# Kernel tuning notes

Measured on AMD Instinct MI355X. Metric: run time of the kernel, lower is better.

Reference implementation:

```python
import jax, jax.numpy as jnp
import numpy as np

EMBED_DIM = 256
N_LEVELS = 4
N_HEADS = 8
N_POINTS = 4
HEAD_DIM = EMBED_DIM // N_HEADS
N_QUERIES = 8192
BATCH = 2
LEVEL_SHAPES = np.array([[128, 128], [64, 64], [32, 32], [16, 16]], dtype=np.int32)
HMAX, WMAX = 128, 128
EPS = 1e-5


def setup_inputs() -> dict:
    key = jax.random.key(0)
    ks = jax.random.split(key, 10)
    scale = 1.0 / np.sqrt(EMBED_DIM)
    query = jax.random.normal(ks[0], (N_QUERIES, EMBED_DIM), jnp.float32)
    xy_reference_points = jax.random.uniform(ks[1], (N_QUERIES, 2), jnp.float32, 0.05, 0.95)
    val = jax.random.normal(ks[2], (BATCH, HMAX, WMAX, N_LEVELS, EMBED_DIM), jnp.float32)
    # zero outside each level's valid support (mimics sparse COO: absent entries read as 0)
    hh = jnp.arange(HMAX)[:, None, None]
    ww = jnp.arange(WMAX)[None, :, None]
    lh = jnp.asarray(LEVEL_SHAPES[:, 0])[None, None, :]
    lw = jnp.asarray(LEVEL_SHAPES[:, 1])[None, None, :]
    mask = ((hh < lh) & (ww < lw)).astype(jnp.float32)
    stacked_value_tensors = val * mask[None, :, :, :, None]
    return {
        "query": query,
        "xy_reference_points": xy_reference_points,
        "stacked_value_tensors": stacked_value_tensors,
        "W_off": (jax.random.normal(ks[3], (EMBED_DIM, N_LEVELS * N_POINTS * N_HEADS * 2)) * scale * 0.1).astype(jnp.float32),
        "b_off": (jax.random.normal(ks[4], (N_LEVELS * N_POINTS * N_HEADS * 2,)) * 0.5).astype(jnp.float32),
        "W_attn": (jax.random.normal(ks[5], (EMBED_DIM, N_LEVELS * N_POINTS * N_HEADS)) * scale).astype(jnp.float32),
        "b_attn": jnp.zeros((N_LEVELS * N_POINTS * N_HEADS,), jnp.float32),
        "W_out": (jax.random.normal(ks[6], (EMBED_DIM, EMBED_DIM)) * scale).astype(jnp.float32),
        "b_out": jnp.zeros((EMBED_DIM,), jnp.float32),
        "batch_offsets": jnp.array([0, N_QUERIES // 2], jnp.int32),
        "spatial_shapes": jnp.asarray(LEVEL_SHAPES, jnp.int32),
    }


def reference(query, xy_reference_points, stacked_value_tensors, W_off, b_off,
              W_attn, b_attn, W_out, b_out, batch_offsets, spatial_shapes):
    Q = query.shape[0]
    # sampling offsets & attention weights (torch Linear with W stored [in,out])
    off = (query @ W_off + b_off).reshape(Q, N_LEVELS, N_POINTS, N_HEADS, 2)
    aw = (query @ W_attn + b_attn).reshape(Q, N_LEVELS * N_POINTS, N_HEADS)
    aw = jax.nn.softmax(aw, axis=1).reshape(Q, N_LEVELS, N_POINTS, N_HEADS)
    # sampling locations: sigmoid(inverse_sigmoid(ref) + offsets), then map (0,1)->(-1,1)
    r = jnp.clip(xy_reference_points, 0.0, 1.0)
    inv = jnp.log(jnp.clip(r, EPS, 1.0) / jnp.clip(1.0 - r, EPS, 1.0))
    loc = jax.nn.sigmoid(inv[:, None, None, None, :] + off) * 2.0 - 1.0  # (Q,L,P,H,2)
    # per-query batch index from batch_offsets (start index per batch element)
    bidx = jnp.searchsorted(batch_offsets, jnp.arange(Q), side="right") - 1  # (Q,)
    b = bidx[:, None, None, None]
    h_sz = spatial_shapes[:, 0].astype(loc.dtype)[None, :, None, None]
    w_sz = spatial_shapes[:, 1].astype(loc.dtype)[None, :, None, None]
    x = ((loc[..., 0] + 1.0) * w_sz - 1.0) / 2.0  # (Q,L,P,H)
    y = ((loc[..., 1] + 1.0) * h_sz - 1.0) / 2.0
    x0 = jnp.floor(x).astype(jnp.int32); x1 = x0 + 1
    y0 = jnp.floor(y).astype(jnp.int32); y1 = y0 + 1
    wcap = (spatial_shapes[:, 1] - 1).astype(jnp.int32)[None, :, None, None]
    hcap = (spatial_shapes[:, 0] - 1).astype(jnp.int32)[None, :, None, None]
    x0 = jnp.clip(x0, 0, wcap); x1 = jnp.clip(x1, 0, wcap)
    y0 = jnp.clip(y0, 0, hcap); y1 = jnp.clip(y1, 0, hcap)
    x0f = x0.astype(x.dtype); x1f = x1.astype(x.dtype)
    y0f = y0.astype(y.dtype); y1f = y1.astype(y.dtype)
    wa = (x1f - x) * (y1f - y)  # pairs with (x0,y0), as in source
    wb = (x1f - x) * (y - y0f)  # (x0,y1)
    wc = (x - x0f) * (y1f - y)  # (x1,y0)
    wd = (x - x0f) * (y - y0f)  # (x1,y1)
    V = stacked_value_tensors.reshape(BATCH, HMAX, WMAX, N_LEVELS, N_HEADS, HEAD_DIM)
    l = jnp.arange(N_LEVELS)[None, :, None, None]
    h = jnp.arange(N_HEADS)[None, None, None, :]
    # NOTE: source indexes (batch, x, y, level, head) -> x indexes the height dim; levels are square
    def g(xi, yi):
        return V[b, xi, yi, l, h]  # (Q,L,P,H,HEAD_DIM)
    sampled = (wa[..., None] * g(x0, y0) + wb[..., None] * g(x0, y1)
               + wc[..., None] * g(x1, y0) + wd[..., None] * g(x1, y1))
    out = jnp.einsum("qlphd,qlph->qhd", sampled, aw).reshape(Q, EMBED_DIM)
    return out @ W_out + b_out
```

## Files before the change

kernel.cpp:

```cpp
#include <hip/hip_runtime.h>
#include <math.h>

#define ED      256
#define NL      4
#define NH      8
#define NP      4
#define HD      32
#define HMAX    128
#define WMAX    128
#define NLP     16
#define NC      128
#define NOFF_AW 384
#define QPB     4
#define BSTRIDE (HMAX*WMAX*NL*ED)
#define XSTRIDE (WMAX*NL*ED)
#define YSTRIDE (NL*ED)
#define RPB     21760
#define PBC     (RPB*256)

typedef __attribute__((ext_vector_type(8))) __fp16   f16x8;
typedef __attribute__((ext_vector_type(4))) __fp16   f16x4;
typedef __attribute__((ext_vector_type(4))) float    f32x4;

__constant__ int LBASE_ROW[4] = {0, 16384, 20480, 21504};

__global__ __launch_bounds__(1024) void msda_prep_kernel(
    const float* __restrict__ V,
    const float* __restrict__ W_off,
    const float* __restrict__ W_attn,
    const float* __restrict__ W_out,
    __fp16* __restrict__ Vc,
    __fp16* __restrict__ WcatT,
    __fp16* __restrict__ WoutT,
    int nb, int nCompact)
{
    const int bid = blockIdx.x;
    const int t   = threadIdx.x;

    if (bid < nCompact) {
        const int r    = bid * 16 + (t >> 6);
        const int lane = t & 63;
        const int h    = lane >> 3;
        const int j4   = lane & 7;
        const int total_rows = nb * RPB;
        if (r < total_rows) {
            const int b  = r / RPB;
            const int rr = r - b * RPB;
            int l;
            if (rr < 16384)      { l = 0; }
            else if (rr < 20480) { l = 1; }
            else if (rr < 21504) { l = 2; }
            else                 { l = 3; }
            const int pos = rr - LBASE_ROW[l];
            const int lsh = 7 - l;
            const int xi  = pos >> lsh;
            const int yi  = pos & ((1 << lsh) - 1);
            const int plane32 = (1 << (2 * lsh)) * 32;
            const float4 src = *(const float4*)&V[(size_t)b * BSTRIDE +
                (size_t)xi * XSTRIDE + (size_t)yi * YSTRIDE + l * ED +
                h * HD + j4 * 4];
            f16x4 d;
            d[0] = (__fp16)src.x; d[1] = (__fp16)src.y;
            d[2] = (__fp16)src.z; d[3] = (__fp16)src.w;
            const size_t dst = (size_t)b * PBC + (size_t)LBASE_ROW[l] * 256 +
                               (size_t)h * plane32 + (size_t)pos * 32 + j4 * 4;
            *(f16x4*)&Vc[dst] = d;
        }
    } else {
        const int idx = (bid - nCompact) * 1024 + t;
        const int t2 = NOFF_AW * ED;
        const int t3 = ED * ED;
        if (idx < t2) {
            int c = idx >> 8, e = idx & 255;
            float v = (c < ED) ? W_off[e * ED + c] : W_attn[e * NC + (c - ED)];
            WcatT[idx] = (__fp16)v;
        } else if (idx < t2 + t3) {
            int i = idx - t2;
            int c = i >> 8, e = i & 255;
            WoutT[i] = (__fp16)W_out[e * ED + c];
        }
    }
}

__global__ __launch_bounds__(256) void gemm_f16_kernel(
    const float*  __restrict__ A,
    const __fp16* __restrict__ BT,
    const float* __restrict__ bias0,
    const float* __restrict__ bias1,
    float* __restrict__ C,
    int M, int NTOT, int bias_split)
{
    const int wave = threadIdx.x >> 6;
    const int lane = threadIdx.x & 63;
    const int gw   = blockIdx.x * 4 + wave;
    const int ngroups = NTOT >> 6;
    const int mg = gw / ngroups, ng = gw % ngroups;
    const int m16 = mg * 16, n64 = ng * 64;
    if (m16 >= M) return;

    const int mrow = lane & 15;
    const int quad = lane >> 4;

    const float4* Arow = (const float4*)(A + (size_t)(m16 + mrow) * 256 + quad * 8);
    const f16x8* B0 = (const f16x8*)(BT + (size_t)(n64 +  0 + mrow) * 256 + quad * 8);
    const f16x8* B1 = (const f16x8*)(BT + (size_t)(n64 + 16 + mrow) * 256 + quad * 8);
    const f16x8* B2 = (const f16x8*)(BT + (size_t)(n64 + 32 + mrow) * 256 + quad * 8);
    const f16x8* B3 = (const f16x8*)(BT + (size_t)(n64 + 48 + mrow) * 256 + quad * 8);

    f32x4 acc0 = {0.f,0.f,0.f,0.f}, acc1 = acc0, acc2 = acc0, acc3 = acc0;
    #pragma unroll
    for (int kb = 0; kb < 8; ++kb) {
        float4 a0 = Arow[kb * 8 + 0];
        float4 a1 = Arow[kb * 8 + 1];
        float av[8] = {a0.x, a0.y, a0.z, a0.w, a1.x, a1.y, a1.z, a1.w};
        f16x8 ah, al;
        #pragma unroll
        for (int j = 0; j < 8; ++j) {
            __fp16 h = (__fp16)av[j];
            ah[j] = h;
            al[j] = (__fp16)(av[j] - (float)h);
        }
        f16x8 b0 = B0[kb * 4], b1 = B1[kb * 4], b2 = B2[kb * 4], b3 = B3[kb * 4];
        acc0 = __builtin_amdgcn_mfma_f32_16x16x32_f16(ah, b0, acc0, 0, 0, 0);
        acc1 = __builtin_amdgcn_mfma_f32_16x16x32_f16(ah, b1, acc1, 0, 0, 0);
        acc2 = __builtin_amdgcn_mfma_f32_16x16x32_f16(ah, b2, acc2, 0, 0, 0);
        acc3 = __builtin_amdgcn_mfma_f32_16x16x32_f16(ah, b3, acc3, 0, 0, 0);
        acc0 = __builtin_amdgcn_mfma_f32_16x16x32_f16(al, b0, acc0, 0, 0, 0);
        acc1 = __builtin_amdgcn_mfma_f32_16x16x32_f16(al, b1, acc1, 0, 0, 0);
        acc2 = __builtin_amdgcn_mfma_f32_16x16x32_f16(al, b2, acc2, 0, 0, 0);
        acc3 = __builtin_amdgcn_mfma_f32_16x16x32_f16(al, b3, acc3, 0, 0, 0);
    }

    const int col = lane & 15;
    f32x4 accs[4] = {acc0, acc1, acc2, acc3};
    #pragma unroll
    for (int i = 0; i < 4; ++i) {
        int n = n64 + i * 16 + col;
        float b = (n < bias_split) ? bias0[n] : bias1[n - bias_split];
        #pragma unroll
        for (int r = 0; r < 4; ++r) {
            int row = m16 + quad * 4 + r;
            C[(size_t)row * NTOT + n] = accs[i][r] + b;
        }
    }
}

__global__ __launch_bounds__(256) void gemm_ff16_kernel(
    const __fp16* __restrict__ A,
    const __fp16* __restrict__ BT,
    const float* __restrict__ bias,
    float* __restrict__ C,
    int M, int NTOT)
{
    const int wave = threadIdx.x >> 6;
    const int lane = threadIdx.x & 63;
    const int gw   = blockIdx.x * 4 + wave;
    const int ngroups = NTOT >> 6;
    const int mg = gw / ngroups, ng = gw % ngroups;
    const int m16 = mg * 16, n64 = ng * 64;
    if (m16 >= M) return;

    const int mrow = lane & 15;
    const int quad = lane >> 4;

    const f16x8* Arow = (const f16x8*)(A + (size_t)(m16 + mrow) * 256 + quad * 8);
    const f16x8* B0 = (const f16x8*)(BT + (size_t)(n64 +  0 + mrow) * 256 + quad * 8);
    const f16x8* B1 = (const f16x8*)(BT + (size_t)(n64 + 16 + mrow) * 256 + quad * 8);
    const f16x8* B2 = (const f16x8*)(BT + (size_t)(n64 + 32 + mrow) * 256 + quad * 8);
    const f16x8* B3 = (const f16x8*)(BT + (size_t)(n64 + 48 + mrow) * 256 + quad * 8);

    f32x4 acc0 = {0.f,0.f,0.f,0.f}, acc1 = acc0, acc2 = acc0, acc3 = acc0;
    #pragma unroll
    for (int kb = 0; kb < 8; ++kb) {
        f16x8 af = Arow[kb * 4];
        acc0 = __builtin_amdgcn_mfma_f32_16x16x32_f16(af, B0[kb * 4], acc0, 0, 0, 0);
        acc1 = __builtin_amdgcn_mfma_f32_16x16x32_f16(af, B1[kb * 4], acc1, 0, 0, 0);
        acc2 = __builtin_amdgcn_mfma_f32_16x16x32_f16(af, B2[kb * 4], acc2, 0, 0, 0);
        acc3 = __builtin_amdgcn_mfma_f32_16x16x32_f16(af, B3[kb * 4], acc3, 0, 0, 0);
    }

    const int col = lane & 15;
    f32x4 accs[4] = {acc0, acc1, acc2, acc3};
    #pragma unroll
    for (int i = 0; i < 4; ++i) {
        int n = n64 + i * 16 + col;
        float b = bias[n];
        #pragma unroll
        for (int r = 0; r < 4; ++r) {
            int row = m16 + quad * 4 + r;
            C[(size_t)row * NTOT + n] = accs[i][r] + b;
        }
    }
}

__global__ __launch_bounds__(256) void msda_sample_kernel(
    const float*  __restrict__ refp,
    const __fp16* __restrict__ Vc,
    const float*  __restrict__ off_aw,
    const int*    __restrict__ batch_off,
    int n_batch,
    __fp16* __restrict__ out_pre,
    int q_total)
{
    __shared__ float  law[QPB][NC];
    __shared__ float2 sminv[QPB][NH];
    __shared__ float2 sref[QPB];
    __shared__ int2   soff[QPB][NC];
    __shared__ float4 swt[QPB][NC];

    const int t  = threadIdx.x;
    const int q0 = blockIdx.x * QPB;

    {
        const int s = t >> 6, c = t & 63;
        const float* row = off_aw + (size_t)(q0 + s) * NOFF_AW + ED;
        law[s][c]      = row[c];
        law[s][c + 64] = row[c + 64];
    }
    __syncthreads();

    if (t < QPB * NH) {
        const int s = t >> 3, h = t & 7;
        float m = -1e30f;
        #pragma unroll
        for (int lp = 0; lp < NLP; ++lp) m = fmaxf(m, law[s][lp * NH + h]);
        float sum = 0.f;
        #pragma unroll
        for (int lp = 0; lp < NLP; ++lp) sum += __expf(law[s][lp * NH + h] - m);
        sminv[s][h] = make_float2(m, 1.f / sum);
    } else if (t < QPB * NH + QPB) {
        const int s = t - QPB * NH;
        const int qid = q0 + s;
        float rx = refp[qid * 2 + 0], ry = refp[qid * 2 + 1];
        rx = fminf(fmaxf(rx, 0.f), 1.f);
        ry = fminf(fmaxf(ry, 0.f), 1.f);
        float ivx = __logf(fmaxf(rx, 1e-5f) / fmaxf(1.f - rx, 1e-5f));
        float ivy = __logf(fmaxf(ry, 1e-5f) / fmaxf(1.f - ry, 1e-5f));
        sref[s] = make_float2(ivx, ivy);
    }
    __syncthreads();

    {
        const int s = t >> 6;
        const int qid = q0 + s;
        int b = 0;
        for (int i = 1; i < n_batch; ++i)
            if (batch_off[i] <= qid) b = i;
        const int cb = b * PBC;
        const float2 iv = sref[s];
        const float* offrow = off_aw + (size_t)qid * NOFF_AW;

        #pragma unroll
        for (int half = 0; half < 2; ++half) {
            const int c = (t & 63) + half * 64;
            const int l = c >> 5;
            const int lsh = 7 - l;
            const int sz  = 1 << lsh;
            const int cap = sz - 1;
            const int h = c & 7;
            const int plane32 = (sz * sz) << 5;

            const float2 mi = sminv[s][h];
            const float a = __expf(law[s][c] - mi.x) * mi.y;

            const float ox = offrow[c * 2 + 0], oy = offrow[c * 2 + 1];
            float lx = 2.f / (1.f + __expf(-(iv.x + ox))) - 1.f;
            float ly = 2.f / (1.f + __expf(-(iv.y + oy))) - 1.f;
            float x = ((lx + 1.f) * (float)sz - 1.f) * 0.5f;
            float y = ((ly + 1.f) * (float)sz - 1.f) * 0.5f;
            int x0 = (int)floorf(x), y0 = (int)floorf(y);
            int x1 = x0 + 1, y1 = y0 + 1;
            x0 = min(max(x0, 0), cap); x1 = min(max(x1, 0), cap);
            y0 = min(max(y0, 0), cap); y1 = min(max(y1, 0), cap);
            float x0f = (float)x0, x1f = (float)x1;
            float y0f = (float)y0, y1f = (float)y1;

            float w00 = a * (x1f - x) * (y1f - y);
            float w01 = a * (x1f - x) * (y - y0f);
            float w10 = a * (x - x0f) * (y1f - y);
            float w11 = a * (x - x0f) * (y - y0f);
            if (y1 == y0) {
                w00 += w01; w01 = 0.f;
                w10 += w11; w11 = 0.f;
            }
            swt[s][c] = make_float4(w00, w01, w10, w11);
            const int lb = cb + (LBASE_ROW[l] << 8) + h * plane32;
            int2 o;
            o.x = lb + (((x0 << lsh) + y0) << 5);
            o.y = lb + (((x1 << lsh) + y0) << 5);
            soff[s][c] = o;
        }
    }
    __syncthreads();

    {
        const int s    = t >> 6;
        const int lane = t & 63;
        const int h    = lane >> 3;
        const int j    = lane & 7;
        const int top  = j >> 2;
        const int blk  = j & 3;

        float acc[8];
        #pragma unroll
        for (int k = 0; k < 8; ++k) acc[k] = 0.f;

        #pragma unroll 4
        for (int lp = 0; lp < NLP; ++lp) {
            const int c = lp * NH + h;
            int2   o = soff[s][c];
            float4 w = swt[s][c];
            f16x8 va = *(const f16x8*)&Vc[o.x + j * 8];
            f16x8 vb = *(const f16x8*)&Vc[o.y + j * 8];
            const float wa = top ? w.y : w.x;
            const float wb = top ? w.w : w.z;
            #pragma unroll
            for (int k = 0; k < 8; ++k)
                acc[k] += wa * (float)va[k] + wb * (float)vb[k];
        }
        #pragma unroll
        for (int k = 0; k < 8; ++k)
            acc[k] += __shfl_xor(acc[k], 4);

        if (top == 0) {
            f16x8 o8;
            #pragma unroll
            for (int k = 0; k < 8; ++k) o8[k] = (__fp16)acc[k];
            *(f16x8*)&out_pre[(size_t)(q0 + s) * ED + h * HD + blk * 8] = o8;
        }
    }
}

extern "C" void kernel_launch(void* const* d_in, const int* in_sizes, int n_in,
                              void* d_out, int out_size, void* d_ws, size_t ws_size,
                              hipStream_t stream) {
    const float* query  = (const float*)d_in[0];
    const float* refp   = (const float*)d_in[1];
    const float* V      = (const float*)d_in[2];
    const float* W_off  = (const float*)d_in[3];
    const float* b_off  = (const float*)d_in[4];
    const float* W_attn = (const float*)d_in[5];
    const float* b_attn = (const float*)d_in[6];
    const float* W_out  = (const float*)d_in[7];
    const float* b_out  = (const float*)d_in[8];
    const int*   boff   = (const int*)d_in[9];
    const int n_batch   = in_sizes[9];
    const int nq        = in_sizes[0] / ED;
    const int nb        = in_sizes[2] / BSTRIDE;
    float* out = (float*)d_out;

    char* ws = (char*)d_ws;
    float*   off_aw  = (float*)ws;
    __fp16*  WcatT   = (__fp16*)(off_aw + (size_t)nq * NOFF_AW);
    __fp16*  WoutT   = WcatT + NOFF_AW * ED;
    __fp16*  out_pre = WoutT + ED * ED;
    __fp16*  Vc      = out_pre + (size_t)nq * ED;

    {
        int nCompact = (nb * RPB + 15) / 16;
        int nWconv   = (NOFF_AW * ED + ED * ED + 1023) / 1024;
        msda_prep_kernel<<<nCompact + nWconv, 1024, 0, stream>>>(
            V, W_off, W_attn, W_out, Vc, WcatT, WoutT, nb, nCompact);
    }
    {
        int waves = (nq / 16) * (NOFF_AW / 64);
        gemm_f16_kernel<<<(waves + 3) / 4, 256, 0, stream>>>(
            query, WcatT, b_off, b_attn, off_aw, nq, NOFF_AW, ED);
    }
    {
        msda_sample_kernel<<<nq / QPB, 256, 0, stream>>>(
            refp, Vc, off_aw, boff, n_batch, out_pre, nq);
    }
    {
        int waves = (nq / 16) * (ED / 64);
        gemm_ff16_kernel<<<(waves + 3) / 4, 256, 0, stream>>>(
            out_pre, WoutT, b_out, out, nq, ED);
    }
}
```

Before: 256.8 us.

## Fuse output projection GEMM into sampling kernel via shared-memory tile

Removes the separate output-projection GEMM kernel. The sampling kernel now processes 8 queries per block with 512 threads, writes the sampled fp16 rows into a 16-row shared tile with the unused rows zeroed, and runs the W_out MFMA directly from shared memory. This drops the global round trip of the intermediate buffer and one launch. In exchange, half of each MFMA tile is padding, and every block re-reads all of W_out from global or cache.

Measured after the change: 259.3 us. About the same (+1.0%).

```diff
diff --git a/kernel.cpp b/kernel.cpp
--- a/kernel.cpp
+++ b/kernel.cpp
@@ -11,7 +11,7 @@
 #define NLP     16
 #define NC      128
 #define NOFF_AW 384
-#define QPB     4
+#define QPB     8
 #define BSTRIDE (HMAX*WMAX*NL*ED)
 #define XSTRIDE (WMAX*NL*ED)
 #define YSTRIDE (NL*ED)
@@ -145,61 +145,15 @@
     }
 }
 
-__global__ __launch_bounds__(256) void gemm_ff16_kernel(
-    const __fp16* __restrict__ A,
-    const __fp16* __restrict__ BT,
-    const float* __restrict__ bias,
-    float* __restrict__ C,
-    int M, int NTOT)
-{
-    const int wave = threadIdx.x >> 6;
-    const int lane = threadIdx.x & 63;
-    const int gw   = blockIdx.x * 4 + wave;
-    const int ngroups = NTOT >> 6;
-    const int mg = gw / ngroups, ng = gw % ngroups;
-    const int m16 = mg * 16, n64 = ng * 64;
-    if (m16 >= M) return;
-
-    const int mrow = lane & 15;
-    const int quad = lane >> 4;
-
-    const f16x8* Arow = (const f16x8*)(A + (size_t)(m16 + mrow) * 256 + quad * 8);
-    const f16x8* B0 = (const f16x8*)(BT + (size_t)(n64 +  0 + mrow) * 256 + quad * 8);
-    const f16x8* B1 = (const f16x8*)(BT + (size_t)(n64 + 16 + mrow) * 256 + quad * 8);
-    const f16x8* B2 = (const f16x8*)(BT + (size_t)(n64 + 32 + mrow) * 256 + quad * 8);
-    const f16x8* B3 = (const f16x8*)(BT + (size_t)(n64 + 48 + mrow) * 256 + quad * 8);
-
-    f32x4 acc0 = {0.f,0.f,0.f,0.f}, acc1 = acc0, acc2 = acc0, acc3 = acc0;
-    #pragma unroll
-    for (int kb = 0; kb < 8; ++kb) {
-        f16x8 af = Arow[kb * 4];
-        acc0 = __builtin_amdgcn_mfma_f32_16x16x32_f16(af, B0[kb * 4], acc0, 0, 0, 0);
-        acc1 = __builtin_amdgcn_mfma_f32_16x16x32_f16(af, B1[kb * 4], acc1, 0, 0, 0);
-        acc2 = __builtin_amdgcn_mfma_f32_16x16x32_f16(af, B2[kb * 4], acc2, 0, 0, 0);
-        acc3 = __builtin_amdgcn_mfma_f32_16x16x32_f16(af, B3[kb * 4], acc3, 0, 0, 0);
-    }
-
-    const int col = lane & 15;
-    f32x4 accs[4] = {acc0, acc1, acc2, acc3};
-    #pragma unroll
-    for (int i = 0; i < 4; ++i) {
-        int n = n64 + i * 16 + col;
-        float b = bias[n];
-        #pragma unroll
-        for (int r = 0; r < 4; ++r) {
-            int row = m16 + quad * 4 + r;
-            C[(size_t)row * NTOT + n] = accs[i][r] + b;
-        }
-    }
-}
-
-__global__ __launch_bounds__(256) void msda_sample_kernel(
+__global__ __launch_bounds__(512) void msda_sample_kernel(
     const float*  __restrict__ refp,
     const __fp16* __restrict__ Vc,
     const float*  __restrict__ off_aw,
     const int*    __restrict__ batch_off,
     int n_batch,
-    __fp16* __restrict__ out_pre,
+    const __fp16* __restrict__ WoutT,
+    const float*  __restrict__ b_out,
+    float* __restrict__ out,
     int q_total)
 {
     __shared__ float  law[QPB][NC];
@@ -207,9 +161,15 @@
     __shared__ float2 sref[QPB];
     __shared__ int2   soff[QPB][NC];
     __shared__ float4 swt[QPB][NC];
+    __shared__ __attribute__((aligned(16))) __fp16 sout[16][ED + 8];
 
     const int t  = threadIdx.x;
     const int q0 = blockIdx.x * QPB;
+
+    if (t < 264) {
+        f16x8 z = {};
+        ((f16x8*)&sout[QPB][0])[t] = z;
+    }
 
     {
         const int s = t >> 6, c = t & 63;
@@ -326,7 +286,40 @@
             f16x8 o8;
             #pragma unroll
             for (int k = 0; k < 8; ++k) o8[k] = (__fp16)acc[k];
-            *(f16x8*)&out_pre[(size_t)(q0 + s) * ED + h * HD + blk * 8] = o8;
+            *(f16x8*)&sout[s][h * HD + blk * 8] = o8;
+        }
+    }
+    __syncthreads();
+
+    {
+        const int w    = t >> 6;
+        const int lane = t & 63;
+        const int mrow = lane & 15;
+        const int quad = lane >> 4;
+
+        const f16x8* B0 = (const f16x8*)(WoutT + (size_t)(w * 32 +  0 + mrow) * 256 + quad * 8);
+        const f16x8* B1 = (const f16x8*)(WoutT + (size_t)(w * 32 + 16 + mrow) * 256 + quad * 8);
+
+        f32x4 acc0 = {0.f,0.f,0.f,0.f}, acc1 = acc0;
+        #pragma unroll
+        for (int kb = 0; kb < 8; ++kb) {
+            f16x8 af = *(const f16x8*)&sout[mrow][quad * 8 + kb * 32];
+            acc0 = __builtin_amdgcn_mfma_f32_16x16x32_f16(af, B0[kb * 4], acc0, 0, 0, 0);
+            acc1 = __builtin_amdgcn_mfma_f32_16x16x32_f16(af, B1[kb * 4], acc1, 0, 0, 0);
+        }
+
+        const int col = lane & 15;
+        f32x4 accs[2] = {acc0, acc1};
+        #pragma unroll
+        for (int i = 0; i < 2; ++i) {
+            int n = w * 32 + i * 16 + col;
+            float bb = b_out[n];
+            #pragma unroll
+            for (int r = 0; r < 4; ++r) {
+                int row = quad * 4 + r;
+                if (row < QPB)
+                    out[(size_t)(q0 + row) * ED + n] = accs[i][r] + bb;
+            }
         }
     }
 }
@@ -353,8 +346,7 @@
     float*   off_aw  = (float*)ws;
     __fp16*  WcatT   = (__fp16*)(off_aw + (size_t)nq * NOFF_AW);
     __fp16*  WoutT   = WcatT + NOFF_AW * ED;
-    __fp16*  out_pre = WoutT + ED * ED;
-    __fp16*  Vc      = out_pre + (size_t)nq * ED;
+    __fp16*  Vc      = WoutT + ED * ED;
 
     {
         int nCompact = (nb * RPB + 15) / 16;
@@ -368,12 +360,7 @@
             query, WcatT, b_off, b_attn, off_aw, nq, NOFF_AW, ED);
     }
     {
-        msda_sample_kernel<<<nq / QPB, 256, 0, stream>>>(
-            refp, Vc, off_aw, boff, n_batch, out_pre, nq);
-    }
-    {
-        int waves = (nq / 16) * (ED / 64);
-        gemm_ff16_kernel<<<(waves + 3) / 4, 256, 0, stream>>>(
-            out_pre, WoutT, b_out, out, nq, ED);
+        msda_sample_kernel<<<nq / QPB, 512, 0, stream>>>(
+            refp, Vc, off_aw, boff, n_batch, WoutT, b_out, out, nq);
     }
 }
```

## Co-schedule offset/attention GEMM with value compaction in one launch

Applied to the files above, without the earlier changes.

Splits weight conversion into its own small kernel, then merges the offset/attention-weight GEMM and the value-tensor fp16 compaction into a single heterogeneous launch. GEMM blocks come first in the grid, so the compute-bound GEMM can overlap with the bandwidth-bound compaction instead of running serially. The cost is an extra tiny launch for the weights, 1024-thread blocks for the GEMM part, and a grid that mixes two workloads.

After: 256.2 us. No clear change (-0.3%).

```diff
diff --git a/kernel.cpp b/kernel.cpp
--- a/kernel.cpp
+++ b/kernel.cpp
@@ -24,22 +24,95 @@
 
 __constant__ int LBASE_ROW[4] = {0, 16384, 20480, 21504};
 
-__global__ __launch_bounds__(1024) void msda_prep_kernel(
-    const float* __restrict__ V,
+__global__ __launch_bounds__(1024) void msda_wconv_kernel(
     const float* __restrict__ W_off,
     const float* __restrict__ W_attn,
     const float* __restrict__ W_out,
+    __fp16* __restrict__ WcatT,
+    __fp16* __restrict__ WoutT)
+{
+    const int idx = blockIdx.x * 1024 + threadIdx.x;
+    const int t2 = NOFF_AW * ED;
+    const int t3 = ED * ED;
+    if (idx < t2) {
+        int c = idx >> 8, e = idx & 255;
+        float v = (c < ED) ? W_off[e * ED + c] : W_attn[e * NC + (c - ED)];
+        WcatT[idx] = (__fp16)v;
+    } else if (idx < t2 + t3) {
+        int i = idx - t2;
+        int c = i >> 8, e = i & 255;
+        WoutT[i] = (__fp16)W_out[e * ED + c];
+    }
+}
+
+__global__ __launch_bounds__(1024) void msda_mix_kernel(
+    const float* __restrict__ V,
     __fp16* __restrict__ Vc,
-    __fp16* __restrict__ WcatT,
-    __fp16* __restrict__ WoutT,
-    int nb, int nCompact)
+    const float* __restrict__ query,
+    const __fp16* __restrict__ WcatT,
+    const float* __restrict__ b_off,
+    const float* __restrict__ b_attn,
+    float* __restrict__ off_aw,
+    int nb, int ngemm, int M)
 {
-    const int bid = blockIdx.x;
-    const int t   = threadIdx.x;
-
-    if (bid < nCompact) {
-        const int r    = bid * 16 + (t >> 6);
-        const int lane = t & 63;
+    const int bid  = blockIdx.x;
+    const int wave = threadIdx.x >> 6;
+    const int lane = threadIdx.x & 63;
+
+    if (bid < ngemm) {
+        const int gw = bid * 16 + wave;
+        const int ngroups = NOFF_AW >> 6;
+        const int mg = gw / ngroups, ng = gw % ngroups;
+        const int m16 = mg * 16, n64 = ng * 64;
+        if (m16 >= M) return;
+
+        const int mrow = lane & 15;
+        const int quad = lane >> 4;
+
+        const float4* Arow = (const float4*)(query + (size_t)(m16 + mrow) * 256 + quad * 8);
+        const f16x8* B0 = (const f16x8*)(WcatT + (size_t)(n64 +  0 + mrow) * 256 + quad * 8);
+        const f16x8* B1 = (const f16x8*)(WcatT + (size_t)(n64 + 16 + mrow) * 256 + quad * 8);
+        const f16x8* B2 = (const f16x8*)(WcatT + (size_t)(n64 + 32 + mrow) * 256 + quad * 8);
+        const f16x8* B3 = (const f16x8*)(WcatT + (size_t)(n64 + 48 + mrow) * 256 + quad * 8);
+
+        f32x4 acc0 = {0.f,0.f,0.f,0.f}, acc1 = acc0, acc2 = acc0, acc3 = acc0;
+        #pragma unroll
+        for (int kb = 0; kb < 8; ++kb) {
+            float4 a0 = Arow[kb * 8 + 0];
+            float4 a1 = Arow[kb * 8 + 1];
+            float av[8] = {a0.x, a0.y, a0.z, a0.w, a1.x, a1.y, a1.z, a1.w};
+            f16x8 ah, al;
+            #pragma unroll
+            for (int j = 0; j < 8; ++j) {
+                __fp16 h = (__fp16)av[j];
+                ah[j] = h;
+                al[j] = (__fp16)(av[j] - (float)h);
+            }
+            f16x8 b0 = B0[kb * 4], b1 = B1[kb * 4], b2 = B2[kb * 4], b3 = B3[kb * 4];
+            acc0 = __builtin_amdgcn_mfma_f32_16x16x32_f16(ah, b0, acc0, 0, 0, 0);
+            acc1 = __builtin_amdgcn_mfma_f32_16x16x32_f16(ah, b1, acc1, 0, 0, 0);
+            acc2 = __builtin_amdgcn_mfma_f32_16x16x32_f16(ah, b2, acc2, 0, 0, 0);
+            acc3 = __builtin_amdgcn_mfma_f32_16x16x32_f16(ah, b3, acc3, 0, 0, 0);
+            acc0 = __builtin_amdgcn_mfma_f32_16x16x32_f16(al, b0, acc0, 0, 0, 0);
+            acc1 = __builtin_amdgcn_mfma_f32_16x16x32_f16(al, b1, acc1, 0, 0, 0);
+            acc2 = __builtin_amdgcn_mfma_f32_16x16x32_f16(al, b2, acc2, 0, 0, 0);
+            acc3 = __builtin_amdgcn_mfma_f32_16x16x32_f16(al, b3, acc3, 0, 0, 0);
+        }
+
+        const int col = lane & 15;
+        f32x4 accs[4] = {acc0, acc1, acc2, acc3};
+        #pragma unroll
+        for (int i = 0; i < 4; ++i) {
+            int n = n64 + i * 16 + col;
+            float b = (n < ED) ? b_off[n] : b_attn[n - ED];
+            #pragma unroll
+            for (int r = 0; r < 4; ++r) {
+                int row = m16 + quad * 4 + r;
+                off_aw[(size_t)row * NOFF_AW + n] = accs[i][r] + b;
+            }
+        }
+    } else {
+        const int r = (bid - ngemm) * 16 + wave;
         const int h    = lane >> 3;
         const int j4   = lane & 7;
         const int total_rows = nb * RPB;
@@ -66,81 +139,143 @@
                                (size_t)h * plane32 + (size_t)pos * 32 + j4 * 4;
             *(f16x4*)&Vc[dst] = d;
         }
-    } else {
-        const int idx = (bid - nCompact) * 1024 + t;
-        const int t2 = NOFF_AW * ED;
-        const int t3 = ED * ED;
-        if (idx < t2) {
-            int c = idx >> 8, e = idx & 255;
-            float v = (c < ED) ? W_off[e * ED + c] : W_attn[e * NC + (c - ED)];
-            WcatT[idx] = (__fp16)v;
-        } else if (idx < t2 + t3) {
-            int i = idx - t2;
-            int c = i >> 8, e = i & 255;
-            WoutT[i] = (__fp16)W_out[e * ED + c];
-        }
-    }
-}
-
-__global__ __launch_bounds__(256) void gemm_f16_kernel(
-    const float*  __restrict__ A,
-    const __fp16* __restrict__ BT,
-    const float* __restrict__ bias0,
-    const float* __restrict__ bias1,
-    float* __restrict__ C,
-    int M, int NTOT, int bias_split)
+    }
+}
+
+__global__ __launch_bounds__(256) void msda_sample_kernel(
+    const float*  __restrict__ refp,
+    const __fp16* __restrict__ Vc,
+    const float*  __restrict__ off_aw,
+    const int*    __restrict__ batch_off,
+    int n_batch,
+    __fp16* __restrict__ out_pre,
+    int q_total)
 {
-    const int wave = threadIdx.x >> 6;
-    const int lane = threadIdx.x & 63;
-    const int gw   = blockIdx.x * 4 + wave;
-    const int ngroups = NTOT >> 6;
-    const int mg = gw / ngroups, ng = gw % ngroups;
-    const int m16 = mg * 16, n64 = ng * 64;
-    if (m16 >= M) return;
-
-    const int mrow = lane & 15;
-    const int quad = lane >> 4;
-
-    const float4* Arow = (const float4*)(A + (size_t)(m16 + mrow) * 256 + quad * 8);
-    const f16x8* B0 = (const f16x8*)(BT + (size_t)(n64 +  0 + mrow) * 256 + quad * 8);
-    const f16x8* B1 = (const f16x8*)(BT + (size_t)(n64 + 16 + mrow) * 256 + quad * 8);
-    const f16x8* B2 = (const f16x8*)(BT + (size_t)(n64 + 32 + mrow) * 256 + quad * 8);
-    const f16x8* B3 = (const f16x8*)(BT + (size_t)(n64 + 48 + mrow) * 256 + quad * 8);
-
-    f32x4 acc0 = {0.f,0.f,0.f,0.f}, acc1 = acc0, acc2 = acc0, acc3 = acc0;
-    #pragma unroll
-    for (int kb = 0; kb < 8; ++kb) {
-        float4 a0 = Arow[kb * 8 + 0];
-        float4 a1 = Arow[kb * 8 + 1];
-        float av[8] = {a0.x, a0.y, a0.z, a0.w, a1.x, a1.y, a1.z, a1.w};
-        f16x8 ah, al;
-        #pragma unroll
-        for (int j = 0; j < 8; ++j) {
-            __fp16 h = (__fp16)av[j];
-            ah[j] = h;
-            al[j] = (__fp16)(av[j] - (float)h);
-        }
-        f16x8 b0 = B0[kb * 4], b1 = B1[kb * 4], b2 = B2[kb * 4], b3 = B3[kb * 4];
-        acc0 = __builtin_amdgcn_mfma_f32_16x16x32_f16(ah, b0, acc0, 0, 0, 0);
-        acc1 = __builtin_amdgcn_mfma_f32_16x16x32_f16(ah, b1, acc1, 0, 0, 0);
-        acc2 = __builtin_amdgcn_mfma_f32_16x16x32_f16(ah, b2, acc2, 0, 0, 0);
-        acc3 = __builtin_amdgcn_mfma_f32_16x16x32_f16(ah, b3, acc3, 0, 0, 0);
-        acc0 = __builtin_amdgcn_mfma_f32_16x16x32_f16(al, b0, acc0, 0, 0, 0);
-        acc1 = __builtin_amdgcn_mfma_f32_16x16x32_f16(al, b1, acc1, 0, 0, 0);
-        acc2 = __builtin_amdgcn_mfma_f32_16x16x32_f16(al, b2, acc2, 0, 0, 0);
-        acc3 = __builtin_amdgcn_mfma_f32_16x16x32_f16(al, b3, acc3, 0, 0, 0);
-    }
-
-    const int col = lane & 15;
-    f32x4 accs[4] = {acc0, acc1, acc2, acc3};
-    #pragma unroll
-    for (int i = 0; i < 4; ++i) {
-        int n = n64 + i * 16 + col;
-        float b = (n < bias_split) ? bias0[n] : bias1[n - bias_split];
-        #pragma unroll
-        for (int r = 0; r < 4; ++r) {
-            int row = m16 + quad * 4 + r;
-            C[(size_t)row * NTOT + n] = accs[i][r] + b;
+    __shared__ float  law[QPB][NC];
+    __shared__ float2 sminv[QPB][NH];
+    __shared__ float2 sref[QPB];
+    __shared__ int2   soff[QPB][NC];
+    __shared__ float4 swt[QPB][NC];
+
+    const int t  = threadIdx.x;
+    const int q0 = blockIdx.x * QPB;
+
+    {
+        const int s = t >> 6, c = t & 63;
+        const float* row = off_aw + (size_t)(q0 + s) * NOFF_AW + ED;
+        law[s][c]      = row[c];
+        law[s][c + 64] = row[c + 64];
+    }
+    __syncthreads();
+
+    if (t < QPB * NH) {
+        const int s = t >> 3, h = t & 7;
+        float m = -1e30f;
+        #pragma unroll
+        for (int lp = 0; lp < NLP; ++lp) m = fmaxf(m, law[s][lp * NH + h]);
+        float sum = 0.f;
+        #pragma unroll
+        for (int lp = 0; lp < NLP; ++lp) sum += __expf(law[s][lp * NH + h] - m);
+        sminv[s][h] = make_float2(m, 1.f / sum);
+    } else if (t < QPB * NH + QPB) {
+        const int s = t - QPB * NH;
+        const int qid = q0 + s;
+        float rx = refp[qid * 2 + 0], ry = refp[qid * 2 + 1];
+        rx = fminf(fmaxf(rx, 0.f), 1.f);
+        ry = fminf(fmaxf(ry, 0.f), 1.f);
+        float ivx = __logf(fmaxf(rx, 1e-5f) / fmaxf(1.f - rx, 1e-5f));
+        float ivy = __logf(fmaxf(ry, 1e-5f) / fmaxf(1.f - ry, 1e-5f));
+        sref[s] = make_float2(ivx, ivy);
+    }
+    __syncthreads();
+
+    {
+        const int s = t >> 6;
+        const int qid = q0 + s;
+        int b = 0;
+        for (int i = 1; i < n_batch; ++i)
+            if (batch_off[i] <= qid) b = i;
+        const int cb = b * PBC;
+        const float2 iv = sref[s];
+        const float* offrow = off_aw + (size_t)qid * NOFF_AW;
+
+        #pragma unroll
+        for (int half = 0; half < 2; ++half) {
+            const int c = (t & 63) + half * 64;
+            const int l = c >> 5;
+            const int lsh = 7 - l;
+            const int sz  = 1 << lsh;
+            const int cap = sz - 1;
+            const int h = c & 7;
+            const int plane32 = (sz * sz) << 5;
+
+            const float2 mi = sminv[s][h];
+            const float a = __expf(law[s][c] - mi.x) * mi.y;
+
+            const float ox = offrow[c * 2 + 0], oy = offrow[c * 2 + 1];
+            float lx = 2.f / (1.f + __expf(-(iv.x + ox))) - 1.f;
+            float ly = 2.f / (1.f + __expf(-(iv.y + oy))) - 1.f;
+            float x = ((lx + 1.f) * (float)sz - 1.f) * 0.5f;
+            float y = ((ly + 1.f) * (float)sz - 1.f) * 0.5f;
+            int x0 = (int)floorf(x), y0 = (int)floorf(y);
+            int x1 = x0 + 1, y1 = y0 + 1;
+            x0 = min(max(x0, 0), cap); x1 = min(max(x1, 0), cap);
+            y0 = min(max(y0, 0), cap); y1 = min(max(y1, 0), cap);
+            float x0f = (float)x0, x1f = (float)x1;
+            float y0f = (float)y0, y1f = (float)y1;
+
+            float w00 = a * (x1f - x) * (y1f - y);
+            float w01 = a * (x1f - x) * (y - y0f);
+            float w10 = a * (x - x0f) * (y1f - y);
+            float w11 = a * (x - x0f) * (y - y0f);
+            if (y1 == y0) {
+                w00 += w01; w01 = 0.f;
+                w10 += w11; w11 = 0.f;
+            }
+            swt[s][c] = make_float4(w00, w01, w10, w11);
+            const int lb = cb + (LBASE_ROW[l] << 8) + h * plane32;
+            int2 o;
+            o.x = lb + (((x0 << lsh) + y0) << 5);
+            o.y = lb + (((x1 << lsh) + y0) << 5);
+            soff[s][c] = o;
+        }
+    }
+    __syncthreads();
+
+    {
+        const int s    = t >> 6;
+        const int lane = t & 63;
+        const int h    = lane >> 3;
+        const int j    = lane & 7;
+        const int top  = j >> 2;
+        const int blk  = j & 3;
+
+        float acc[8];
+        #pragma unroll
+        for (int k = 0; k < 8; ++k) acc[k] = 0.f;
+
+        #pragma unroll 4
+        for (int lp = 0; lp < NLP; ++lp) {
+            const int c = lp * NH + h;
+            int2   o = soff[s][c];
+            float4 w = swt[s][c];
+            f16x8 va = *(const f16x8*)&Vc[o.x + j * 8];
+            f16x8 vb = *(const f16x8*)&Vc[o.y + j * 8];
+            const float wa = top ? w.y : w.x;
+            const float wb = top ? w.w : w.z;
+            #pragma unroll
+            for (int k = 0; k < 8; ++k)
+                acc[k] += wa * (float)va[k] + wb * (float)vb[k];
+        }
+        #pragma unroll
+        for (int k = 0; k < 8; ++k)
+            acc[k] += __shfl_xor(acc[k], 4);
+
+        if (top == 0) {
+            f16x8 o8;
+            #pragma unroll
+            for (int k = 0; k < 8; ++k) o8[k] = (__fp16)acc[k];
+            *(f16x8*)&out_pre[(size_t)(q0 + s) * ED + h * HD + blk * 8] = o8;
         }
     }
 }
@@ -189,144 +324,6 @@
         for (int r = 0; r < 4; ++r) {
             int row = m16 + quad * 4 + r;
             C[(size_t)row * NTOT + n] = accs[i][r] + b;
-        }
-    }
-}
-
-__global__ __launch_bounds__(256) void msda_sample_kernel(
-    const float*  __restrict__ refp,
-    const __fp16* __restrict__ Vc,
-    const float*  __restrict__ off_aw,
-    const int*    __restrict__ batch_off,
-    int n_batch,
-    __fp16* __restrict__ out_pre,
-    int q_total)
-{
-    __shared__ float  law[QPB][NC];
-    __shared__ float2 sminv[QPB][NH];
-    __shared__ float2 sref[QPB];
-    __shared__ int2   soff[QPB][NC];
-    __shared__ float4 swt[QPB][NC];
-
-    const int t  = threadIdx.x;
-    const int q0 = blockIdx.x * QPB;
-
-    {
-        const int s = t >> 6, c = t & 63;
-        const float* row = off_aw + (size_t)(q0 + s) * NOFF_AW + ED;
-        law[s][c]      = row[c];
-        law[s][c + 64] = row[c + 64];
-    }
-    __syncthreads();
-
-    if (t < QPB * NH) {
-        const int s = t >> 3, h = t & 7;
-        float m = -1e30f;
-        #pragma unroll
-        for (int lp = 0; lp < NLP; ++lp) m = fmaxf(m, law[s][lp * NH + h]);
-        float sum = 0.f;
-        #pragma unroll
-        for (int lp = 0; lp < NLP; ++lp) sum += __expf(law[s][lp * NH + h] - m);
-        sminv[s][h] = make_float2(m, 1.f / sum);
-    } else if (t < QPB * NH + QPB) {
-        const int s = t - QPB * NH;
-        const int qid = q0 + s;
-        float rx = refp[qid * 2 + 0], ry = refp[qid * 2 + 1];
-        rx = fminf(fmaxf(rx, 0.f), 1.f);
-        ry = fminf(fmaxf(ry, 0.f), 1.f);
-        float ivx = __logf(fmaxf(rx, 1e-5f) / fmaxf(1.f - rx, 1e-5f));
-        float ivy = __logf(fmaxf(ry, 1e-5f) / fmaxf(1.f - ry, 1e-5f));
-        sref[s] = make_float2(ivx, ivy);
-    }
-    __syncthreads();
-
-    {
-        const int s = t >> 6;
-        const int qid = q0 + s;
-        int b = 0;
-        for (int i = 1; i < n_batch; ++i)
-            if (batch_off[i] <= qid) b = i;
-        const int cb = b * PBC;
-        const float2 iv = sref[s];
-        const float* offrow = off_aw + (size_t)qid * NOFF_AW;
-
-        #pragma unroll
-        for (int half = 0; half < 2; ++half) {
-            const int c = (t & 63) + half * 64;
-            const int l = c >> 5;
-            const int lsh = 7 - l;
-            const int sz  = 1 << lsh;
-            const int cap = sz - 1;
-            const int h = c & 7;
-            const int plane32 = (sz * sz) << 5;
-
-            const float2 mi = sminv[s][h];
-            const float a = __expf(law[s][c] - mi.x) * mi.y;
-
-            const float ox = offrow[c * 2 + 0], oy = offrow[c * 2 + 1];
-            float lx = 2.f / (1.f + __expf(-(iv.x + ox))) - 1.f;
-            float ly = 2.f / (1.f + __expf(-(iv.y + oy))) - 1.f;
-            float x = ((lx + 1.f) * (float)sz - 1.f) * 0.5f;
-            float y = ((ly + 1.f) * (float)sz - 1.f) * 0.5f;
-            int x0 = (int)floorf(x), y0 = (int)floorf(y);
-            int x1 = x0 + 1, y1 = y0 + 1;
-            x0 = min(max(x0, 0), cap); x1 = min(max(x1, 0), cap);
-            y0 = min(max(y0, 0), cap); y1 = min(max(y1, 0), cap);
-            float x0f = (float)x0, x1f = (float)x1;
-            float y0f = (float)y0, y1f = (float)y1;
-
-            float w00 = a * (x1f - x) * (y1f - y);
-            float w01 = a * (x1f - x) * (y - y0f);
-            float w10 = a * (x - x0f) * (y1f - y);
-            float w11 = a * (x - x0f) * (y - y0f);
-            if (y1 == y0) {
-                w00 += w01; w01 = 0.f;
-                w10 += w11; w11 = 0.f;
-            }
-            swt[s][c] = make_float4(w00, w01, w10, w11);
-            const int lb = cb + (LBASE_ROW[l] << 8) + h * plane32;
-            int2 o;
-            o.x = lb + (((x0 << lsh) + y0) << 5);
-            o.y = lb + (((x1 << lsh) + y0) << 5);
-            soff[s][c] = o;
-        }
-    }
-    __syncthreads();
-
-    {
-        const int s    = t >> 6;
-        const int lane = t & 63;
-        const int h    = lane >> 3;
-        const int j    = lane & 7;
-        const int top  = j >> 2;
-        const int blk  = j & 3;
-
-        float acc[8];
-        #pragma unroll
-        for (int k = 0; k < 8; ++k) acc[k] = 0.f;
-
-        #pragma unroll 4
-        for (int lp = 0; lp < NLP; ++lp) {
-            const int c = lp * NH + h;
-            int2   o = soff[s][c];
-            float4 w = swt[s][c];
-            f16x8 va = *(const f16x8*)&Vc[o.x + j * 8];
-            f16x8 vb = *(const f16x8*)&Vc[o.y + j * 8];
-            const float wa = top ? w.y : w.x;
-            const float wb = top ? w.w : w.z;
-            #pragma unroll
-            for (int k = 0; k < 8; ++k)
-                acc[k] += wa * (float)va[k] + wb * (float)vb[k];
-        }
-        #pragma unroll
-        for (int k = 0; k < 8; ++k)
-            acc[k] += __shfl_xor(acc[k], 4);
-
-        if (top == 0) {
-            f16x8 o8;
-            #pragma unroll
-            for (int k = 0; k < 8; ++k) o8[k] = (__fp16)acc[k];
-            *(f16x8*)&out_pre[(size_t)(q0 + s) * ED + h * HD + blk * 8] = o8;
         }
     }
 }
@@ -357,15 +354,15 @@
     __fp16*  Vc      = out_pre + (size_t)nq * ED;
 
     {
+        int nWconv = (NOFF_AW * ED + ED * ED + 1023) / 1024;
+        msda_wconv_kernel<<<nWconv, 1024, 0, stream>>>(
+            W_off, W_attn, W_out, WcatT, WoutT);
+    }
+    {
+        int ngemm    = ((nq / 16) * (NOFF_AW / 64) + 15) / 16;
         int nCompact = (nb * RPB + 15) / 16;
-        int nWconv   = (NOFF_AW * ED + ED * ED + 1023) / 1024;
-        msda_prep_kernel<<<nCompact + nWconv, 1024, 0, stream>>>(
-            V, W_off, W_attn, W_out, Vc, WcatT, WoutT, nb, nCompact);
-    }
-    {
-        int waves = (nq / 16) * (NOFF_AW / 64);
-        gemm_f16_kernel<<<(waves + 3) / 4, 256, 0, stream>>>(
-            query, WcatT, b_off, b_attn, off_aw, nq, NOFF_AW, ED);
+        msda_mix_kernel<<<ngemm + nCompact, 1024, 0, stream>>>(
+            V, Vc, query, WcatT, b_off, b_attn, off_aw, nb, ngemm, nq);
     }
     {
         msda_sample_kernel<<<nq / QPB, 256, 0, stream>>>(
```
